# Kernel tuning notes

Hardware: AMD Instinct MI355X
Metric: run time of the kernel (lower is better)

Reference implementation:

```python
import jax, jax.numpy as jnp
import numpy as np

USER_COUNT = 100000
ITEM_COUNT = 50000
N_NODES = USER_COUNT + ITEM_COUNT
NNZ = 4800000
EMB = 64
BATCH = 4096


def setup_inputs() -> dict:
    key = jax.random.key(0)
    k1, k2, k3, k4, k5, k6, k7 = jax.random.split(key, 7)
    return {
        "user_emb": jax.random.normal(k1, (USER_COUNT, EMB), dtype=jnp.float32),
        "item_emb": jax.random.normal(k2, (ITEM_COUNT, EMB), dtype=jnp.float32),
        "adj_vals": jax.random.uniform(k3, (NNZ,), dtype=jnp.float32),
        "adj_row": jax.random.randint(k4, (NNZ,), 0, N_NODES, dtype=jnp.int64),
        "adj_col": jax.random.randint(k5, (NNZ,), 0, N_NODES, dtype=jnp.int64),
        "users": jax.random.randint(k6, (BATCH,), 0, USER_COUNT, dtype=jnp.int64),
        "items": jax.random.randint(k7, (BATCH,), 0, ITEM_COUNT, dtype=jnp.int64),
        "n_layers": 3,
    }


def _spmm(adj_row, adj_col, adj_vals, x):
    # sparse (N,N) @ dense (N,D): gather source rows, scale by edge values, scatter-add to dest
    msgs = adj_vals[:, None] * x[adj_col]  # [nnz, D]
    return jax.ops.segment_sum(msgs, adj_row, num_segments=N_NODES)


def reference(user_emb, item_emb, adj_vals, adj_row, adj_col, users, items, n_layers):
    ego = jnp.concatenate([user_emb, item_emb], axis=0)  # [N, D]
    for _ in range(n_layers):
        ego = _spmm(adj_row, adj_col, adj_vals, ego)
    user_all = ego[:USER_COUNT]
    item_all = ego[USER_COUNT:]
    return (user_all[users], item_all[items])
```

## Files before the change

### kernel.cpp

```cpp
#include <hip/hip_runtime.h>
#include <hip/hip_bf16.h>

#define USER_COUNT 100000
#define ITEM_COUNT 50000
#define N_NODES    150000
#define EMB        64
#define BATCH      4096

#define NFINE      586
#define FSHIFT     8
#define STRIDE     8960
#define TILE_E     6400
#define NBSTRIDE   768

__device__ inline unsigned short f2bf_raw(float f) {
    __hip_bfloat16 h = __float2bfloat16(f);
    unsigned short u; __builtin_memcpy(&u, &h, 2); return u;
}

__global__ __launch_bounds__(512) void count_kernel(
        const int* __restrict__ rows, int* __restrict__ counts, int nnz) {
    __shared__ int cnt[NFINE];
    const int b = blockIdx.x, t = threadIdx.x;
    for (int f = t; f < NFINE; f += 512) cnt[f] = 0;
    __syncthreads();
    const int s = b * TILE_E, e = min(s + TILE_E, nnz);
    for (int i = s + t; i < e; i += 512)
        atomicAdd(&cnt[rows[i] >> FSHIFT], 1);
    __syncthreads();
    for (int f = t; f < NFINE; f += 512)
        counts[f * NBSTRIDE + b] = cnt[f];
}

__global__ __launch_bounds__(1024) void scan_offs(
        const int* __restrict__ counts, int* __restrict__ offs,
        int* __restrict__ tot, int nblk) {
    __shared__ int s[1024];
    const int f = blockIdx.x, t = threadIdx.x;
    const int c = (t < nblk) ? counts[f * NBSTRIDE + t] : 0;
    s[t] = c;
    __syncthreads();
    for (int o = 1; o < 1024; o <<= 1) {
        int v = (t >= o) ? s[t - o] : 0;
        __syncthreads();
        s[t] += v;
        __syncthreads();
    }
    if (t < nblk) offs[f * NBSTRIDE + t] = s[t] - c;
    if (t == 1023) tot[f] = s[1023];
}

__global__ __launch_bounds__(512) void partition_kernel(
        const float* __restrict__ vals,
        const int* __restrict__ rows,
        const int* __restrict__ cols,
        const int* __restrict__ offs,
        uint2* __restrict__ fine, int nnz) {
    __shared__ uint2 buf[TILE_E];
    __shared__ int   cnt[NFINE];
    __shared__ int   sloff[NFINE + 1];
    __shared__ int   gb[NFINE];
    __shared__ int   sscan[512];
    const int b = blockIdx.x, t = threadIdx.x;
    const int sbeg = b * TILE_E, send = min(sbeg + TILE_E, nnz);
    const int n = send - sbeg;

    for (int f = t; f < NFINE; f += 512) {
        cnt[f] = 0;
        gb[f] = f * STRIDE + offs[f * NBSTRIDE + b];
    }
    __syncthreads();
    for (int i = sbeg + t; i < send; i += 512)
        atomicAdd(&cnt[rows[i] >> FSHIFT], 1);
    __syncthreads();
    int c0 = (2 * t < NFINE) ? cnt[2 * t] : 0;
    int c1 = (2 * t + 1 < NFINE) ? cnt[2 * t + 1] : 0;
    sscan[t] = c0 + c1;
    __syncthreads();
    for (int o = 1; o < 512; o <<= 1) {
        int v = (t >= o) ? sscan[t - o] : 0;
        __syncthreads();
        sscan[t] += v;
        __syncthreads();
    }
    int base = (t == 0) ? 0 : sscan[t - 1];
    if (2 * t < NFINE) sloff[2 * t] = base;
    if (2 * t + 1 < NFINE) sloff[2 * t + 1] = base + c0;
    if (t == 511) sloff[NFINE] = sscan[511];
    __syncthreads();
    for (int f = t; f < NFINE; f += 512) cnt[f] = sloff[f];
    __syncthreads();
    for (int i = sbeg + t; i < send; i += 512) {
        int r = rows[i];
        int f = r >> FSHIFT;
        int pos = atomicAdd(&cnt[f], 1);
        buf[pos] = make_uint2(__float_as_uint(vals[i]),
                              (unsigned)cols[i] | ((unsigned)(r & 255) << 18));
    }
    __syncthreads();
    for (int idx = t; idx < n; idx += 512) {
        int lo = 0, hi = NFINE;
        while (hi - lo > 1) {
            int mid = (lo + hi) >> 1;
            if (sloff[mid] <= idx) lo = mid; else hi = mid;
        }
        fine[gb[lo] + (idx - sloff[lo])] = buf[idx];
    }
}

__global__ __launch_bounds__(256) void bucket_sort_kernel(
        const uint2* __restrict__ fine,
        const int* __restrict__ tot,
        float2* __restrict__ perm,
        uint2* __restrict__ rp) {
    __shared__ int hist[256];
    __shared__ int off[256];
    __shared__ int cur[256];
    const int f    = blockIdx.x;
    const int tid  = threadIdx.x;
    const int n    = min(tot[f], STRIDE);
    const int base = f * STRIDE;
    const uint2* src = fine + base;

    hist[tid] = 0;
    __syncthreads();
    for (int k = tid; k < n; k += 256)
        atomicAdd(&hist[(src[k].y >> 18) & 255], 1);
    __syncthreads();
    if (tid == 0) {
        int acc = 0;
        for (int j = 0; j < 256; ++j) { off[j] = acc; acc += hist[j]; }
    }
    __syncthreads();
    cur[tid] = off[tid];
    int row = (f << FSHIFT) + tid;
    if (row < N_NODES)
        rp[row] = make_uint2(base + off[tid], base + off[tid] + hist[tid]);
    __syncthreads();
    for (int k = tid; k < n; k += 256) {
        uint2 e = src[k];
        int lrow = (e.y >> 18) & 255;
        int pos = base + atomicAdd(&cur[lrow], 1);
        perm[pos] = make_float2(__uint_as_float(e.x),
                                __int_as_float((int)(e.y & 0x3FFFFu)));
    }
}

__global__ void to_bf16(const float4* __restrict__ ue,
                        const float4* __restrict__ ie,
                        uint2* __restrict__ xh) {
    int i = blockIdx.x * blockDim.x + threadIdx.x;
    const int n4 = (N_NODES * EMB) / 4;
    const int u4 = (USER_COUNT * EMB) / 4;
    if (i >= n4) return;
    float4 fv = (i < u4) ? ue[i] : ie[i - u4];
    uint2 o;
    o.x = (unsigned int)f2bf_raw(fv.x) | ((unsigned int)f2bf_raw(fv.y) << 16);
    o.y = (unsigned int)f2bf_raw(fv.z) | ((unsigned int)f2bf_raw(fv.w) << 16);
    xh[i] = o;
}

#define ACC8(U, W)                                      \
    a0 += (W) * __uint_as_float((U).x << 16);           \
    a1 += (W) * __uint_as_float((U).x & 0xffff0000u);   \
    a2 += (W) * __uint_as_float((U).y << 16);           \
    a3 += (W) * __uint_as_float((U).y & 0xffff0000u);   \
    a4 += (W) * __uint_as_float((U).z << 16);           \
    a5 += (W) * __uint_as_float((U).z & 0xffff0000u);   \
    a6 += (W) * __uint_as_float((U).w << 16);           \
    a7 += (W) * __uint_as_float((U).w & 0xffff0000u);

__global__ void spmm_bf16(const uint2* __restrict__ rp,
                          const float2* __restrict__ perm,
                          const unsigned short* __restrict__ xh,
                          unsigned short* __restrict__ yh) {
    int wid  = (blockIdx.x * blockDim.x + threadIdx.x) >> 6;
    int lane = threadIdx.x & 63;
    int g    = lane >> 3;
    int s    = lane & 7;
    int r    = (wid << 3) + g;
    if (r >= N_NODES) return;

    uint2 be = rp[r];
    int beg = (int)be.x, end = (int)be.y;

    const uint4* xv = (const uint4*)xh;
    float a0 = 0.f, a1 = 0.f, a2 = 0.f, a3 = 0.f;
    float a4 = 0.f, a5 = 0.f, a6 = 0.f, a7 = 0.f;

    int j = beg;
    for (; j + 7 < end; j += 8) {
        float2 e0 = perm[j];
        float2 e1 = perm[j + 1];
        float2 e2 = perm[j + 2];
        float2 e3 = perm[j + 3];
        float2 e4 = perm[j + 4];
        float2 e5 = perm[j + 5];
        float2 e6 = perm[j + 6];
        float2 e7 = perm[j + 7];
        uint4 u0 = xv[(((long long)__float_as_int(e0.y)) << 3) + s];
        uint4 u1 = xv[(((long long)__float_as_int(e1.y)) << 3) + s];
        uint4 u2 = xv[(((long long)__float_as_int(e2.y)) << 3) + s];
        uint4 u3 = xv[(((long long)__float_as_int(e3.y)) << 3) + s];
        uint4 u4 = xv[(((long long)__float_as_int(e4.y)) << 3) + s];
        uint4 u5 = xv[(((long long)__float_as_int(e5.y)) << 3) + s];
        uint4 u6 = xv[(((long long)__float_as_int(e6.y)) << 3) + s];
        uint4 u7 = xv[(((long long)__float_as_int(e7.y)) << 3) + s];
        ACC8(u0, e0.x) ACC8(u1, e1.x) ACC8(u2, e2.x) ACC8(u3, e3.x)
        ACC8(u4, e4.x) ACC8(u5, e5.x) ACC8(u6, e6.x) ACC8(u7, e7.x)
    }
    for (; j < end; ++j) {
        float2 e = perm[j];
        uint4 u = xv[(((long long)__float_as_int(e.y)) << 3) + s];
        ACC8(u, e.x)
    }

    uint4 o;
    o.x = (unsigned)f2bf_raw(a0) | ((unsigned)f2bf_raw(a1) << 16);
    o.y = (unsigned)f2bf_raw(a2) | ((unsigned)f2bf_raw(a3) << 16);
    o.z = (unsigned)f2bf_raw(a4) | ((unsigned)f2bf_raw(a5) << 16);
    o.w = (unsigned)f2bf_raw(a6) | ((unsigned)f2bf_raw(a7) << 16);
    ((uint4*)yh)[(((long long)r) << 3) + s] = o;
}

__global__ void spmm_batch_kernel(const uint2* __restrict__ rp,
                                  const float2* __restrict__ perm,
                                  const unsigned short* __restrict__ xh,
                                  const int* __restrict__ users,
                                  const int* __restrict__ items,
                                  float4* __restrict__ out) {
    int wid  = (blockIdx.x * blockDim.x + threadIdx.x) >> 6;
    int lane = threadIdx.x & 63;
    int g    = lane >> 3;
    int s    = lane & 7;
    int b    = (wid << 3) + g;
    if (b >= 2 * BATCH) return;
    int node = (b < BATCH) ? users[b] : (USER_COUNT + items[b - BATCH]);

    uint2 be = rp[node];
    int beg = (int)be.x, end = (int)be.y;

    const uint4* xv = (const uint4*)xh;
    float a0 = 0.f, a1 = 0.f, a2 = 0.f, a3 = 0.f;
    float a4 = 0.f, a5 = 0.f, a6 = 0.f, a7 = 0.f;

    int j = beg;
    for (; j + 3 < end; j += 4) {
        float2 e0 = perm[j];
        float2 e1 = perm[j + 1];
        float2 e2 = perm[j + 2];
        float2 e3 = perm[j + 3];
        uint4 u0 = xv[(((long long)__float_as_int(e0.y)) << 3) + s];
        uint4 u1 = xv[(((long long)__float_as_int(e1.y)) << 3) + s];
        uint4 u2 = xv[(((long long)__float_as_int(e2.y)) << 3) + s];
        uint4 u3 = xv[(((long long)__float_as_int(e3.y)) << 3) + s];
        ACC8(u0, e0.x) ACC8(u1, e1.x) ACC8(u2, e2.x) ACC8(u3, e3.x)
    }
    for (; j < end; ++j) {
        float2 e = perm[j];
        uint4 u = xv[(((long long)__float_as_int(e.y)) << 3) + s];
        ACC8(u, e.x)
    }

    out[(size_t)b * 16 + 2 * s]     = make_float4(a0, a1, a2, a3);
    out[(size_t)b * 16 + 2 * s + 1] = make_float4(a4, a5, a6, a7);
}

extern "C" void kernel_launch(void* const* d_in, const int* in_sizes, int n_in,
                              void* d_out, int out_size, void* d_ws, size_t ws_size,
                              hipStream_t stream) {
    const float* user_emb = (const float*)d_in[0];
    const float* item_emb = (const float*)d_in[1];
    const float* adj_vals = (const float*)d_in[2];
    const int*   adj_row  = (const int*)d_in[3];
    const int*   adj_col  = (const int*)d_in[4];
    const int*   users    = (const int*)d_in[5];
    const int*   items    = (const int*)d_in[6];

    const int nnz  = in_sizes[2];
    const int nblk = (nnz + TILE_E - 1) / TILE_E;

    const size_t region = (size_t)NFINE * STRIDE + 1024;

    char* p = (char*)d_ws;
    uint2* fine = (uint2*)p;
    unsigned short* xh_a = (unsigned short*)p;
    unsigned short* xh_b = xh_a + (size_t)N_NODES * EMB;
    p += region * sizeof(uint2);
    float2* perm = (float2*)p;
    p += region * sizeof(float2);
    uint2* rp = (uint2*)p;
    p += (size_t)(N_NODES + 16) * sizeof(uint2);
    int* counts = (int*)p;  p += (size_t)NFINE * NBSTRIDE * sizeof(int);
    int* offs   = (int*)p;  p += (size_t)NFINE * NBSTRIDE * sizeof(int);
    int* tot    = (int*)p;

    count_kernel<<<nblk, 512, 0, stream>>>(adj_row, counts, nnz);
    scan_offs<<<NFINE, 1024, 0, stream>>>(counts, offs, tot, nblk);
    partition_kernel<<<nblk, 512, 0, stream>>>(adj_vals, adj_row, adj_col,
                                               offs, fine, nnz);
    bucket_sort_kernel<<<NFINE, 256, 0, stream>>>(fine, tot, perm, rp);

    const int n4 = (N_NODES * EMB) / 4;
    to_bf16<<<(n4 + 255) / 256, 256, 0, stream>>>((const float4*)user_emb,
                                                  (const float4*)item_emb,
                                                  (uint2*)xh_a);

    const int spmm_blocks = (N_NODES / 8 + 3) / 4;
    spmm_bf16<<<spmm_blocks, 256, 0, stream>>>(rp, perm, xh_a, xh_b);
    spmm_bf16<<<spmm_blocks, 256, 0, stream>>>(rp, perm, xh_b, xh_a);
    spmm_batch_kernel<<<(2 * BATCH / 8) / 4, 256, 0, stream>>>(
        rp, perm, xh_a, users, items, (float4*)d_out);
}
```

Before: 440.8 us.

## Store bucket ids in partition, shrink tile, nontemporal edge loads in SpMM

The partition kernel now records each edge's fine bucket id in shared memory, so the scatter step no longer needs a per-element binary search over bucket offsets. The edge tile shrinks and the block stride grows to match, which changes shared-memory use and the number of partition blocks. The SpMM kernels read the packed (weight, col) edge stream with nontemporal loads so it does not push the reused embedding rows out of cache. The main SpMM loop unroll drops from 8 to 4, which may lower memory-level parallelism.

```diff
diff --git a/kernel.cpp b/kernel.cpp
--- a/kernel.cpp
+++ b/kernel.cpp
@@ -10,8 +10,8 @@
 #define NFINE      586
 #define FSHIFT     8
 #define STRIDE     8960
-#define TILE_E     6400
-#define NBSTRIDE   768
+#define TILE_E     5120
+#define NBSTRIDE   960
 
 __device__ inline unsigned short f2bf_raw(float f) {
     __hip_bfloat16 h = __float2bfloat16(f);
@@ -56,11 +56,12 @@
         const int* __restrict__ cols,
         const int* __restrict__ offs,
         uint2* __restrict__ fine, int nnz) {
-    __shared__ uint2 buf[TILE_E];
-    __shared__ int   cnt[NFINE];
-    __shared__ int   sloff[NFINE + 1];
-    __shared__ int   gb[NFINE];
-    __shared__ int   sscan[512];
+    __shared__ uint2          buf[TILE_E];
+    __shared__ unsigned short bid[TILE_E];
+    __shared__ int            cnt[NFINE];
+    __shared__ int            sloff[NFINE + 1];
+    __shared__ int            gb[NFINE];
+    __shared__ int            sscan[512];
     const int b = blockIdx.x, t = threadIdx.x;
     const int sbeg = b * TILE_E, send = min(sbeg + TILE_E, nnz);
     const int n = send - sbeg;
@@ -96,15 +97,12 @@
         int pos = atomicAdd(&cnt[f], 1);
         buf[pos] = make_uint2(__float_as_uint(vals[i]),
                               (unsigned)cols[i] | ((unsigned)(r & 255) << 18));
+        bid[pos] = (unsigned short)f;
     }
     __syncthreads();
     for (int idx = t; idx < n; idx += 512) {
-        int lo = 0, hi = NFINE;
-        while (hi - lo > 1) {
-            int mid = (lo + hi) >> 1;
-            if (sloff[mid] <= idx) lo = mid; else hi = mid;
-        }
-        fine[gb[lo] + (idx - sloff[lo])] = buf[idx];
+        int f = bid[idx];
+        fine[gb[f] + (idx - sloff[f])] = buf[idx];
     }
 }
 
@@ -170,6 +168,13 @@
     a6 += (W) * __uint_as_float((U).w << 16);           \
     a7 += (W) * __uint_as_float((U).w & 0xffff0000u);
 
+__device__ inline void perm_nt(const float2* p, float* wv, int* cv) {
+    unsigned long long u = __builtin_nontemporal_load(
+        (const unsigned long long*)p);
+    *wv = __uint_as_float((unsigned)(u & 0xffffffffu));
+    *cv = (int)(u >> 32);
+}
+
 __global__ void spmm_bf16(const uint2* __restrict__ rp,
                           const float2* __restrict__ perm,
                           const unsigned short* __restrict__ xh,
@@ -189,30 +194,24 @@
     float a4 = 0.f, a5 = 0.f, a6 = 0.f, a7 = 0.f;
 
     int j = beg;
-    for (; j + 7 < end; j += 8) {
-        float2 e0 = perm[j];
-        float2 e1 = perm[j + 1];
-        float2 e2 = perm[j + 2];
-        float2 e3 = perm[j + 3];
-        float2 e4 = perm[j + 4];
-        float2 e5 = perm[j + 5];
-        float2 e6 = perm[j + 6];
-        float2 e7 = perm[j + 7];
-        uint4 u0 = xv[(((long long)__float_as_int(e0.y)) << 3) + s];
-        uint4 u1 = xv[(((long long)__float_as_int(e1.y)) << 3) + s];
-        uint4 u2 = xv[(((long long)__float_as_int(e2.y)) << 3) + s];
-        uint4 u3 = xv[(((long long)__float_as_int(e3.y)) << 3) + s];
-        uint4 u4 = xv[(((long long)__float_as_int(e4.y)) << 3) + s];
-        uint4 u5 = xv[(((long long)__float_as_int(e5.y)) << 3) + s];
-        uint4 u6 = xv[(((long long)__float_as_int(e6.y)) << 3) + s];
-        uint4 u7 = xv[(((long long)__float_as_int(e7.y)) << 3) + s];
-        ACC8(u0, e0.x) ACC8(u1, e1.x) ACC8(u2, e2.x) ACC8(u3, e3.x)
-        ACC8(u4, e4.x) ACC8(u5, e5.x) ACC8(u6, e6.x) ACC8(u7, e7.x)
+    for (; j + 3 < end; j += 4) {
+        float w0, w1, w2, w3;
+        int   c0, c1, c2, c3;
+        perm_nt(perm + j,     &w0, &c0);
+        perm_nt(perm + j + 1, &w1, &c1);
+        perm_nt(perm + j + 2, &w2, &c2);
+        perm_nt(perm + j + 3, &w3, &c3);
+        uint4 u0 = xv[(((long long)c0) << 3) + s];
+        uint4 u1 = xv[(((long long)c1) << 3) + s];
+        uint4 u2 = xv[(((long long)c2) << 3) + s];
+        uint4 u3 = xv[(((long long)c3) << 3) + s];
+        ACC8(u0, w0) ACC8(u1, w1) ACC8(u2, w2) ACC8(u3, w3)
     }
     for (; j < end; ++j) {
-        float2 e = perm[j];
-        uint4 u = xv[(((long long)__float_as_int(e.y)) << 3) + s];
-        ACC8(u, e.x)
+        float w; int c;
+        perm_nt(perm + j, &w, &c);
+        uint4 u = xv[(((long long)c) << 3) + s];
+        ACC8(u, w)
     }
 
     uint4 o;
@@ -246,20 +245,23 @@
 
     int j = beg;
     for (; j + 3 < end; j += 4) {
-        float2 e0 = perm[j];
-        float2 e1 = perm[j + 1];
-        float2 e2 = perm[j + 2];
-        float2 e3 = perm[j + 3];
-        uint4 u0 = xv[(((long long)__float_as_int(e0.y)) << 3) + s];
-        uint4 u1 = xv[(((long long)__float_as_int(e1.y)) << 3) + s];
-        uint4 u2 = xv[(((long long)__float_as_int(e2.y)) << 3) + s];
-        uint4 u3 = xv[(((long long)__float_as_int(e3.y)) << 3) + s];
-        ACC8(u0, e0.x) ACC8(u1, e1.x) ACC8(u2, e2.x) ACC8(u3, e3.x)
+        float w0, w1, w2, w3;
+        int   c0, c1, c2, c3;
+        perm_nt(perm + j,     &w0, &c0);
+        perm_nt(perm + j + 1, &w1, &c1);
+        perm_nt(perm + j + 2, &w2, &c2);
+        perm_nt(perm + j + 3, &w3, &c3);
+        uint4 u0 = xv[(((long long)c0) << 3) + s];
+        uint4 u1 = xv[(((long long)c1) << 3) + s];
+        uint4 u2 = xv[(((long long)c2) << 3) + s];
+        uint4 u3 = xv[(((long long)c3) << 3) + s];
+        ACC8(u0, w0) ACC8(u1, w1) ACC8(u2, w2) ACC8(u3, w3)
     }
     for (; j < end; ++j) {
-        float2 e = perm[j];
-        uint4 u = xv[(((long long)__float_as_int(e.y)) << 3) + s];
-        ACC8(u, e.x)
+        float w; int c;
+        perm_nt(perm + j, &w, &c);
+        uint4 u = xv[(((long long)c) << 3) + s];
+        ACC8(u, w)
     }
 
     out[(size_t)b * 16 + 2 * s]     = make_float4(a0, a1, a2, a3);
```

Measured after the change: 459.4 us. 1.04x slower.
